# Performance work log

Measured on AMD Instinct MI355X. Metric: run time of the kernel, lower is better.

## Reference

```python
import jax, jax.numpy as jnp
import numpy as np

N_STEPS = 128        # params['n_steps']
NOISE_SCALE = 0.01   # params['noise_scale']
DIMS_X = 16
HID = 512
BATCH = 32768
DIMS_IN = 2 * DIMS_X + 1  # cond_x1=True: cat([t, x_t, x_1])


def _linear_init(key, fan_in, fan_out):
    # torch nn.Linear default: U(-1/sqrt(fan_in), 1/sqrt(fan_in))
    bound = 1.0 / np.sqrt(fan_in)
    kw, kb = jax.random.split(key)
    w = jax.random.uniform(kw, (fan_in, fan_out), jnp.float32, -bound, bound)
    b = jax.random.uniform(kb, (fan_out,), jnp.float32, -bound, bound)
    return w, b


def setup_inputs() -> dict:
    key = jax.random.key(0)
    ks = jax.random.split(key, 6)
    w0, b0 = _linear_init(ks[0], DIMS_IN, HID)
    w1, b1 = _linear_init(ks[1], HID, HID)
    w2, b2 = _linear_init(ks[2], HID, HID)
    w3, b3 = _linear_init(ks[3], HID, HID)
    w4, b4 = _linear_init(ks[4], HID, DIMS_X)
    x_1 = jax.random.normal(ks[5], (BATCH, DIMS_X), jnp.float32)
    return {"x_1": x_1, "w0": w0, "b0": b0, "w1": w1, "b1": b1,
            "w2": w2, "b2": b2, "w3": w3, "b3": b3, "w4": w4, "b4": b4}


def reference(x_1, w0, b0, w1, b1, w2, b2, w3, b3, w4, b4):
    dtype = x_1.dtype
    steps = jnp.linspace(1.0, 0.0, N_STEPS).astype(dtype)
    t_arr = steps[:-1]       # t
    tprev_arr = steps[1:]    # tprev (< t)
    noise_key = jax.random.key(42)
    ones_col = jnp.ones((x_1.shape[0], 1), dtype)

    def net(t, x_t):
        h = jnp.concatenate([t * ones_col, x_t, x_1], axis=-1)  # [B, 2*Dx+1]
        for w, b in ((w0, b0), (w1, b1), (w2, b2), (w3, b3)):
            h = jax.nn.relu(h @ w + b)
        return h @ w4 + b4  # [B, Dx]

    def body(x_t, inp):
        t, tprev, i = inp
        drift = net(t, x_t)
        pred_x0 = x_t - t * drift
        x_new = (t - tprev) / t * pred_x0 + tprev / t * x_t
        noise = jax.random.normal(jax.random.fold_in(noise_key, i), x_t.shape, dtype)
        x_new = x_new + jnp.sqrt(NOISE_SCALE * tprev * (t - tprev) / t) * noise
        return x_new, None

    x0 = jax.lax.stop_gradient(x_1)  # x_t = x_1.detach()
    x_final, _ = jax.lax.scan(body, x0, (t_arr, tprev_arr, jnp.arange(N_STEPS - 1)))
    return x_final
```

## Files before the change

kernel.cpp:

```cpp
#include <hip/hip_runtime.h>

typedef _Float16 f16;
typedef __attribute__((ext_vector_type(4))) _Float16 f16x4;
typedef __attribute__((ext_vector_type(8))) _Float16 f16x8;
typedef __attribute__((ext_vector_type(4))) float f32x4;
typedef __attribute__((ext_vector_type(16))) float f32x16;

#define HID 512
#define DIMS_X 16
#define NSTEPS 127
#define BM 128
#define BATCH 32768

#define OFF_W0 0
#define OFF_W1 32768
#define OFF_W2 (32768 + 262144)
#define OFF_W3 (32768 + 2 * 262144)
#define OFF_W4 (32768 + 3 * 262144)

__global__ void pack_w_kernel(const float* __restrict__ w, f16* __restrict__ out,
                              int K, int Kpad, int N) {
    int idx = blockIdx.x * blockDim.x + threadIdx.x;
    if (idx >= Kpad * N) return;
    int k = idx / N, n = idx - k * N;
    float v = (k < K) ? w[k * N + n] : 0.0f;
    out[(((k >> 3) * N) + n) * 8 + (k & 7)] = (f16)v;
}

__global__ void pack_w0_kernel(const float* __restrict__ w, f16* __restrict__ out) {
    int idx = blockIdx.x * blockDim.x + threadIdx.x;
    if (idx >= 64 * HID) return;
    int kn = idx / HID, n = idx - kn * HID;
    float v;
    if (kn < 32) v = w[(kn + 1) * HID + n];
    else if (kn == 32) v = w[n];
    else v = 0.0f;
    out[(((kn >> 3) * HID) + n) * 8 + (kn & 7)] = (f16)v;
}

__device__ __forceinline__ unsigned rotl32(unsigned x, int r) {
    return (x << r) | (x >> (32 - r));
}

__device__ __forceinline__ void threefry2x32(unsigned k0, unsigned k1,
                                             unsigned c0, unsigned c1,
                                             unsigned& o0, unsigned& o1) {
    unsigned ks2 = k0 ^ k1 ^ 0x1BD11BDAu;
    unsigned x0 = c0 + k0, x1 = c1 + k1;
#define TF_R(rot) { x0 += x1; x1 = rotl32(x1, rot); x1 ^= x0; }
    TF_R(13) TF_R(15) TF_R(26) TF_R(6)
    x0 += k1;  x1 += ks2 + 1u;
    TF_R(17) TF_R(29) TF_R(16) TF_R(24)
    x0 += ks2; x1 += k0 + 2u;
    TF_R(13) TF_R(15) TF_R(26) TF_R(6)
    x0 += k0;  x1 += k1 + 3u;
    TF_R(17) TF_R(29) TF_R(16) TF_R(24)
    x0 += k1;  x1 += ks2 + 4u;
    TF_R(13) TF_R(15) TF_R(26) TF_R(6)
    x0 += ks2; x1 += k0 + 5u;
#undef TF_R
    o0 = x0; o1 = x1;
}

__device__ __forceinline__ float erfinv_xla(float x) {
    float w = -log1pf(-x * x);
    float p;
    if (w < 5.0f) {
        w = w - 2.5f;
        p = 2.81022636e-08f;
        p = fmaf(p, w, 3.43273939e-07f);
        p = fmaf(p, w, -3.5233877e-06f);
        p = fmaf(p, w, -4.39150654e-06f);
        p = fmaf(p, w, 0.00021858087f);
        p = fmaf(p, w, -0.00125372503f);
        p = fmaf(p, w, -0.00417768164f);
        p = fmaf(p, w, 0.246640727f);
        p = fmaf(p, w, 1.50140941f);
    } else {
        w = sqrtf(w) - 3.0f;
        p = -0.000200214257f;
        p = fmaf(p, w, 0.000100950558f);
        p = fmaf(p, w, 0.00134934322f);
        p = fmaf(p, w, -0.00367342844f);
        p = fmaf(p, w, 0.00573950773f);
        p = fmaf(p, w, -0.0076224613f);
        p = fmaf(p, w, 0.00943887047f);
        p = fmaf(p, w, 1.00167406f);
        p = fmaf(p, w, 2.83297682f);
    }
    return p * x;
}

__device__ __forceinline__ unsigned lds_off(int row, int colByte) {
    return (unsigned)(row * 1024 + (colByte ^ ((row & 31) << 4)));
}

#define KC_BODY(kc, wc, wn, bc, bn, NCHUNK)                                           \
    {                                                                                 \
        if ((kc) + 1 < (NCHUNK)) {                                                    \
            const f16* wk = wbase + (size_t)((kc) + 1) * (2 * HID * 8);               \
            wn[0] = *(const f16x8*)(wk);                                              \
            wn[1] = *(const f16x8*)(wk + 256);                                        \
            _Pragma("unroll")                                                         \
            for (int tb = 0; tb < 4; ++tb)                                            \
                bn[tb] = *(const f16x8*)((const char*)act +                           \
                    lds_off(tb * 32 + l31, ((kc) + 1) * 32 + kh * 16));               \
        }                                                                             \
        _Pragma("unroll")                                                             \
        for (int t = 0; t < 2; ++t)                                                   \
            _Pragma("unroll")                                                         \
            for (int tb = 0; tb < 4; ++tb)                                            \
                acc[t][tb] = __builtin_amdgcn_mfma_f32_32x32x16_f16(                  \
                    wc[t], bc[tb], acc[t][tb], 0, 0, 0);                              \
    }

template <int NCHUNK>
__device__ __forceinline__ void layer_swapped(f16* act, const f16* __restrict__ Wp,
                                              const float* bias_l,
                                              int wv, int l31, int kh) {
    f32x16 acc[2][4];
#pragma unroll
    for (int t = 0; t < 2; ++t) {
        f32x4 bq0 = *(const f32x4*)(bias_l + wv * 64 + t * 32 + 0 + kh * 4);
        f32x4 bq1 = *(const f32x4*)(bias_l + wv * 64 + t * 32 + 8 + kh * 4);
        f32x4 bq2 = *(const f32x4*)(bias_l + wv * 64 + t * 32 + 16 + kh * 4);
        f32x4 bq3 = *(const f32x4*)(bias_l + wv * 64 + t * 32 + 24 + kh * 4);
        f32x16 bv;
#pragma unroll
        for (int r = 0; r < 4; ++r) {
            bv[r] = bq0[r]; bv[4 + r] = bq1[r]; bv[8 + r] = bq2[r]; bv[12 + r] = bq3[r];
        }
#pragma unroll
        for (int tb = 0; tb < 4; ++tb) acc[t][tb] = bv;
    }

    const f16* wbase = Wp + ((size_t)kh * HID + wv * 64 + l31) * 8;
    f16x8 wA[2], wB[2], bA[4], bB[4];
    wA[0] = *(const f16x8*)(wbase);
    wA[1] = *(const f16x8*)(wbase + 256);
#pragma unroll
    for (int tb = 0; tb < 4; ++tb)
        bA[tb] = *(const f16x8*)((const char*)act + lds_off(tb * 32 + l31, kh * 16));

#pragma unroll 1
    for (int kp = 0; kp < NCHUNK / 2; ++kp) {
        KC_BODY(2 * kp, wA, wB, bA, bB, NCHUNK)
        KC_BODY(2 * kp + 1, wB, wA, bB, bA, NCHUNK)
    }

    __syncthreads();
#pragma unroll
    for (int t = 0; t < 2; ++t)
#pragma unroll
        for (int tb = 0; tb < 4; ++tb) {
            int b = tb * 32 + l31;
#pragma unroll
            for (int q = 0; q < 4; ++q) {
                f16x4 v;
#pragma unroll
                for (int r = 0; r < 4; ++r)
                    v[r] = (f16)fmaxf(acc[t][tb][4 * q + r], 0.0f);
                int nb = (wv * 64 + t * 32 + q * 8 + kh * 4) * 2;
                *(f16x4*)((char*)act + lds_off(b, nb)) = v;
            }
        }
    __syncthreads();
}

__global__ __launch_bounds__(512, 2) void didi_main(
    const float* __restrict__ x1g,
    const float* __restrict__ b0g, const float* __restrict__ b1g,
    const float* __restrict__ b2g, const float* __restrict__ b3g,
    const float* __restrict__ b4g,
    const f16* __restrict__ wsp,
    float* __restrict__ outg) {
    __shared__ __align__(16) f16 act[BM * HID];
    __shared__ __align__(16) float bias_lds[4 * HID];

    const f16* W0p = wsp + OFF_W0;
    const f16* W1p = wsp + OFF_W1;
    const f16* W2p = wsp + OFF_W2;
    const f16* W3p = wsp + OFF_W3;
    const f16* W4p = wsp + OFF_W4;

    const int tid = threadIdx.x;
    const int wv = tid >> 6;
    const int ln = tid & 63;
    const int l31 = ln & 31;
    const int kh = ln >> 5;
    const int lk = ln >> 4;
    const int lc = ln & 15;
    const int rowBase = blockIdx.x * BM;

    for (int o = tid; o < HID; o += 512) {
        bias_lds[o] = b0g[o];
        bias_lds[HID + o] = b1g[o];
        bias_lds[2 * HID + o] = b2g[o];
        bias_lds[3 * HID + o] = b3g[o];
    }
    f32x4 bias4v = *(const f32x4*)(b4g + lk * 4);

    {
        f16x8 z = {};
        for (int o = tid; o < (BM * HID) / 8; o += 512)
            *(f16x8*)(act + o * 8) = z;
    }
    __syncthreads();

    f32x4 xr, x1r;
    {
        int grow = rowBase + wv * 16 + lc;
        x1r = *(const f32x4*)(x1g + grow * DIMS_X + lk * 4);
        xr = x1r;
        int lrow = wv * 16 + lc;
        f16x4 xf, x1f;
#pragma unroll
        for (int r = 0; r < 4; ++r) { xf[r] = (f16)xr[r]; x1f[r] = (f16)x1r[r]; }
        *(f16x4*)((char*)act + lds_off(lrow, lk * 8)) = xf;
        *(f16x4*)((char*)act + lds_off(lrow, 32 + lk * 8)) = x1f;
        if (lk == 0)
            *(f16*)((char*)act + lds_off(lrow, 64)) = (f16)1.0f;
    }
    __syncthreads();

    const float dstep = -1.0f / 127.0f;

#pragma unroll 1
    for (int i = 0; i < NSTEPS; ++i) {
        layer_swapped<4>(act, W0p, bias_lds, wv, l31, kh);
        layer_swapped<32>(act, W1p, bias_lds + HID, wv, l31, kh);
        layer_swapped<32>(act, W2p, bias_lds + 2 * HID, wv, l31, kh);
        layer_swapped<32>(act, W3p, bias_lds + 3 * HID, wv, l31, kh);

        float t  = 1.0f + (float)i * dstep;
        float tp = (i == NSTEPS - 1) ? 0.0f : 1.0f + (float)(i + 1) * dstep;

        {
            f32x4 acc4 = bias4v;
#pragma unroll 4
            for (int kc = 0; kc < 16; ++kc) {
                f16x8 w4fr = *(const f16x8*)(W4p + ((size_t)(kc * 4 + lk) * 16 + lc) * 8);
                f16x8 afr = *(const f16x8*)((const char*)act + lds_off(wv * 16 + lc, kc * 64 + lk * 16));
                acc4 = __builtin_amdgcn_mfma_f32_16x16x32_f16(w4fr, afr, acc4, 0, 0, 0);
            }
            float ca = (t - tp) / t;
            float cb = tp / t;
            float sig = sqrtf(((0.01f * tp) * (t - tp)) / t);
            unsigned fk0, fk1;
            threefry2x32(0u, 42u, 0u, (unsigned)i, fk0, fk1);
            int grow = rowBase + wv * 16 + lc;
            int lrow = wv * 16 + lc;
            f16x4 xf, x1f;
#pragma unroll
            for (int r = 0; r < 4; ++r) {
                float drift = acc4[r];
                unsigned flat = (unsigned)grow * 16u + (unsigned)(lk * 4 + r);
                unsigned o0, o1;
                threefry2x32(fk0, fk1, 0u, flat, o0, o1);
                unsigned bits = o0 ^ o1;
                float u01 = __uint_as_float((bits >> 9) | 0x3f800000u) - 1.0f;
                float u = u01 * 2.0f + (-0.99999994f);
                u = fmaxf(-0.99999994f, u);
                float nz = 1.4142135623730951f * erfinv_xla(u);
                float x = xr[r];
                float pred = x - t * drift;
                float xn = ca * pred + cb * x;
                xn = xn + sig * nz;
                xr[r] = xn;
                xf[r] = (f16)xn;
                x1f[r] = (f16)x1r[r];
            }
            *(f16x4*)((char*)act + lds_off(lrow, lk * 8)) = xf;
            *(f16x4*)((char*)act + lds_off(lrow, 32 + lk * 8)) = x1f;
            if (lk == 0)
                *(f16*)((char*)act + lds_off(lrow, 64)) = (f16)tp;
        }
        __syncthreads();
    }

    {
        int grow = rowBase + wv * 16 + lc;
        *(f32x4*)(outg + grow * DIMS_X + lk * 4) = xr;
    }
}

extern "C" void kernel_launch(void* const* d_in, const int* in_sizes, int n_in,
                              void* d_out, int out_size, void* d_ws, size_t ws_size,
                              hipStream_t stream) {
    const float* x1 = (const float*)d_in[0];
    const float* w0 = (const float*)d_in[1];
    const float* b0 = (const float*)d_in[2];
    const float* w1 = (const float*)d_in[3];
    const float* b1 = (const float*)d_in[4];
    const float* w2 = (const float*)d_in[5];
    const float* b2 = (const float*)d_in[6];
    const float* w3 = (const float*)d_in[7];
    const float* b3 = (const float*)d_in[8];
    const float* w4 = (const float*)d_in[9];
    const float* b4 = (const float*)d_in[10];
    f16* ws = (f16*)d_ws;

    hipLaunchKernelGGL(pack_w0_kernel, dim3(128), dim3(256), 0, stream, w0, ws + OFF_W0);
    hipLaunchKernelGGL(pack_w_kernel, dim3(1024), dim3(256), 0, stream, w1, ws + OFF_W1, 512, 512, 512);
    hipLaunchKernelGGL(pack_w_kernel, dim3(1024), dim3(256), 0, stream, w2, ws + OFF_W2, 512, 512, 512);
    hipLaunchKernelGGL(pack_w_kernel, dim3(1024), dim3(256), 0, stream, w3, ws + OFF_W3, 512, 512, 512);
    hipLaunchKernelGGL(pack_w_kernel, dim3(32), dim3(256), 0, stream, w4, ws + OFF_W4, 512, 512, 16);

    hipLaunchKernelGGL(didi_main, dim3(BATCH / BM), dim3(512), 0, stream,
                       x1, b0, b1, b2, b3, b4, (const f16*)ws, (float*)d_out);
}
```

Measured before the change: 6.268 ms.

## Overlap layer epilogue with own-chunk MMAs and stagger K order per wave

Each wave writes its ReLU outputs into the shared activation buffer. Without waiting at a barrier, it then runs the next layer's MMAs on the four K-chunks it just produced, using weights loaded before the epilogue. Only after that does it synchronise and process the remaining chunks in a wave-rotated order. This hides part of the epilogue and barrier latency behind tensor-core work and spreads LDS and weight accesses across waves; the output layer uses the same pattern. Activation fragments are no longer double-buffered in registers, which may expose LDS latency inside the main loop.

```diff
diff --git a/kernel.cpp b/kernel.cpp
--- a/kernel.cpp
+++ b/kernel.cpp
@@ -95,30 +95,26 @@
     return (unsigned)(row * 1024 + (colByte ^ ((row & 31) << 4)));
 }
 
-#define KC_BODY(kc, wc, wn, bc, bn, NCHUNK)                                           \
-    {                                                                                 \
-        if ((kc) + 1 < (NCHUNK)) {                                                    \
-            const f16* wk = wbase + (size_t)((kc) + 1) * (2 * HID * 8);               \
-            wn[0] = *(const f16x8*)(wk);                                              \
-            wn[1] = *(const f16x8*)(wk + 256);                                        \
-            _Pragma("unroll")                                                         \
-            for (int tb = 0; tb < 4; ++tb)                                            \
-                bn[tb] = *(const f16x8*)((const char*)act +                           \
-                    lds_off(tb * 32 + l31, ((kc) + 1) * 32 + kh * 16));               \
-        }                                                                             \
-        _Pragma("unroll")                                                             \
-        for (int t = 0; t < 2; ++t)                                                   \
-            _Pragma("unroll")                                                         \
-            for (int tb = 0; tb < 4; ++tb)                                            \
-                acc[t][tb] = __builtin_amdgcn_mfma_f32_32x32x16_f16(                  \
-                    wc[t], bc[tb], acc[t][tb], 0, 0, 0);                              \
-    }
-
-template <int NCHUNK>
-__device__ __forceinline__ void layer_swapped(f16* act, const f16* __restrict__ Wp,
-                                              const float* bias_l,
-                                              int wv, int l31, int kh) {
-    f32x16 acc[2][4];
+__device__ __forceinline__ void kc_mfma8(f32x16 (&acc)[2][4], const f16* act,
+                                         const f16x8& w0, const f16x8& w1,
+                                         int kc, int l31, int kh) {
+    unsigned colPart = (unsigned)((kc * 32 + kh * 16) ^ (l31 << 4));
+    f16x8 b0 = *(const f16x8*)((const char*)act + (unsigned)((0 * 32 + l31) * 1024) + colPart);
+    f16x8 b1 = *(const f16x8*)((const char*)act + (unsigned)((1 * 32 + l31) * 1024) + colPart);
+    f16x8 b2 = *(const f16x8*)((const char*)act + (unsigned)((2 * 32 + l31) * 1024) + colPart);
+    f16x8 b3 = *(const f16x8*)((const char*)act + (unsigned)((3 * 32 + l31) * 1024) + colPart);
+    acc[0][0] = __builtin_amdgcn_mfma_f32_32x32x16_f16(w0, b0, acc[0][0], 0, 0, 0);
+    acc[0][1] = __builtin_amdgcn_mfma_f32_32x32x16_f16(w0, b1, acc[0][1], 0, 0, 0);
+    acc[0][2] = __builtin_amdgcn_mfma_f32_32x32x16_f16(w0, b2, acc[0][2], 0, 0, 0);
+    acc[0][3] = __builtin_amdgcn_mfma_f32_32x32x16_f16(w0, b3, acc[0][3], 0, 0, 0);
+    acc[1][0] = __builtin_amdgcn_mfma_f32_32x32x16_f16(w1, b0, acc[1][0], 0, 0, 0);
+    acc[1][1] = __builtin_amdgcn_mfma_f32_32x32x16_f16(w1, b1, acc[1][1], 0, 0, 0);
+    acc[1][2] = __builtin_amdgcn_mfma_f32_32x32x16_f16(w1, b2, acc[1][2], 0, 0, 0);
+    acc[1][3] = __builtin_amdgcn_mfma_f32_32x32x16_f16(w1, b3, acc[1][3], 0, 0, 0);
+}
+
+__device__ __forceinline__ void init_acc(f32x16 (&acc)[2][4], const float* bias_l,
+                                         int wv, int kh) {
 #pragma unroll
     for (int t = 0; t < 2; ++t) {
         f32x4 bq0 = *(const f32x4*)(bias_l + wv * 64 + t * 32 + 0 + kh * 4);
@@ -133,22 +129,10 @@
 #pragma unroll
         for (int tb = 0; tb < 4; ++tb) acc[t][tb] = bv;
     }
-
-    const f16* wbase = Wp + ((size_t)kh * HID + wv * 64 + l31) * 8;
-    f16x8 wA[2], wB[2], bA[4], bB[4];
-    wA[0] = *(const f16x8*)(wbase);
-    wA[1] = *(const f16x8*)(wbase + 256);
-#pragma unroll
-    for (int tb = 0; tb < 4; ++tb)
-        bA[tb] = *(const f16x8*)((const char*)act + lds_off(tb * 32 + l31, kh * 16));
-
-#pragma unroll 1
-    for (int kp = 0; kp < NCHUNK / 2; ++kp) {
-        KC_BODY(2 * kp, wA, wB, bA, bB, NCHUNK)
-        KC_BODY(2 * kp + 1, wB, wA, bB, bA, NCHUNK)
-    }
-
-    __syncthreads();
+}
+
+__device__ __forceinline__ void epi_relu(f32x16 (&acc)[2][4], f16* act,
+                                         int wv, int l31, int kh) {
 #pragma unroll
     for (int t = 0; t < 2; ++t)
 #pragma unroll
@@ -164,7 +148,52 @@
                 *(f16x4*)((char*)act + lds_off(b, nb)) = v;
             }
         }
-    __syncthreads();
+}
+
+__device__ __forceinline__ void load_w4(f16x8 (&wE)[8], const f16* __restrict__ Wp,
+                                        int wv4, int l31, int kh) {
+    const f16* wbase = Wp + ((size_t)kh * HID + wv4 * 16 + l31) * 8;
+#pragma unroll
+    for (int j = 0; j < 4; ++j) {
+        const f16* wk = wbase + (size_t)(wv4 + j) * 8192;
+        wE[2 * j] = *(const f16x8*)wk;
+        wE[2 * j + 1] = *(const f16x8*)(wk + 256);
+    }
+}
+
+__device__ __forceinline__ void early4(f32x16 (&acc)[2][4], const f16* act,
+                                       const f16x8 (&wE)[8], int wv4, int l31, int kh) {
+#pragma unroll
+    for (int j = 0; j < 4; ++j)
+        kc_mfma8(acc, act, wE[2 * j], wE[2 * j + 1], wv4 + j, l31, kh);
+}
+
+__device__ __forceinline__ void hidden_main(f32x16 (&acc)[2][4], const f16* act,
+                                            const f16* __restrict__ Wp,
+                                            int wv4, int l31, int kh) {
+    const f16* wbase = Wp + ((size_t)kh * HID + wv4 * 16 + l31) * 8;
+    f16x8 wA0, wA1, wB0, wB1;
+    {
+        int kc = (wv4 + 4) & 31;
+        const f16* wk = wbase + (size_t)kc * 8192;
+        wA0 = *(const f16x8*)wk; wA1 = *(const f16x8*)(wk + 256);
+    }
+#pragma unroll 1
+    for (int kp = 0; kp < 14; ++kp) {
+        int j0 = 4 + 2 * kp;
+        int kc1 = (wv4 + j0 + 1) & 31;
+        {
+            const f16* wk = wbase + (size_t)kc1 * 8192;
+            wB0 = *(const f16x8*)wk; wB1 = *(const f16x8*)(wk + 256);
+        }
+        kc_mfma8(acc, act, wA0, wA1, (wv4 + j0) & 31, l31, kh);
+        int kc2 = (wv4 + j0 + 2) & 31;
+        {
+            const f16* wk = wbase + (size_t)kc2 * 8192;
+            wA0 = *(const f16x8*)wk; wA1 = *(const f16x8*)(wk + 256);
+        }
+        kc_mfma8(acc, act, wB0, wB1, kc1, l31, kh);
+    }
 }
 
 __global__ __launch_bounds__(512, 2) void didi_main(
@@ -190,6 +219,8 @@
     const int kh = ln >> 5;
     const int lk = ln >> 4;
     const int lc = ln & 15;
+    const int wv4 = wv * 4;
+    const int wv2 = wv * 2;
     const int rowBase = blockIdx.x * BM;
 
     for (int o = tid; o < HID; o += 512) {
@@ -224,25 +255,65 @@
     __syncthreads();
 
     const float dstep = -1.0f / 127.0f;
+    f32x16 acc[2][4];
+    f16x8 wE[8];
 
 #pragma unroll 1
     for (int i = 0; i < NSTEPS; ++i) {
-        layer_swapped<4>(act, W0p, bias_lds, wv, l31, kh);
-        layer_swapped<32>(act, W1p, bias_lds + HID, wv, l31, kh);
-        layer_swapped<32>(act, W2p, bias_lds + 2 * HID, wv, l31, kh);
-        layer_swapped<32>(act, W3p, bias_lds + 3 * HID, wv, l31, kh);
+        init_acc(acc, bias_lds, wv, kh);
+        {
+            const f16* wbase = W0p + ((size_t)kh * HID + wv4 * 16 + l31) * 8;
+#pragma unroll
+            for (int kc = 0; kc < 4; ++kc) {
+                const f16* wk = wbase + (size_t)kc * 8192;
+                f16x8 w0 = *(const f16x8*)wk, w1 = *(const f16x8*)(wk + 256);
+                kc_mfma8(acc, act, w0, w1, kc, l31, kh);
+            }
+        }
+        __syncthreads();
+        load_w4(wE, W1p, wv4, l31, kh);
+        epi_relu(acc, act, wv, l31, kh);
+        init_acc(acc, bias_lds + HID, wv, kh);
+        early4(acc, act, wE, wv4, l31, kh);
+        __syncthreads();
+        hidden_main(acc, act, W1p, wv4, l31, kh);
+        __syncthreads();
+        load_w4(wE, W2p, wv4, l31, kh);
+        epi_relu(acc, act, wv, l31, kh);
+        init_acc(acc, bias_lds + 2 * HID, wv, kh);
+        early4(acc, act, wE, wv4, l31, kh);
+        __syncthreads();
+        hidden_main(acc, act, W2p, wv4, l31, kh);
+        __syncthreads();
+        load_w4(wE, W3p, wv4, l31, kh);
+        epi_relu(acc, act, wv, l31, kh);
+        init_acc(acc, bias_lds + 3 * HID, wv, kh);
+        early4(acc, act, wE, wv4, l31, kh);
+        __syncthreads();
+        hidden_main(acc, act, W3p, wv4, l31, kh);
+        __syncthreads();
+        epi_relu(acc, act, wv, l31, kh);
 
         float t  = 1.0f + (float)i * dstep;
         float tp = (i == NSTEPS - 1) ? 0.0f : 1.0f + (float)(i + 1) * dstep;
 
+        f32x4 acc4 = bias4v;
+#pragma unroll
+        for (int j = 0; j < 2; ++j) {
+            int kc = wv2 + j;
+            f16x8 w4fr = *(const f16x8*)(W4p + ((size_t)(kc * 4 + lk) * 16 + lc) * 8);
+            f16x8 afr = *(const f16x8*)((const char*)act + lds_off(wv * 16 + lc, kc * 64 + lk * 16));
+            acc4 = __builtin_amdgcn_mfma_f32_16x16x32_f16(w4fr, afr, acc4, 0, 0, 0);
+        }
+        __syncthreads();
+#pragma unroll
+        for (int j = 2; j < 16; ++j) {
+            int kc = wv2 + j; if (kc >= 16) kc -= 16;
+            f16x8 w4fr = *(const f16x8*)(W4p + ((size_t)(kc * 4 + lk) * 16 + lc) * 8);
+            f16x8 afr = *(const f16x8*)((const char*)act + lds_off(wv * 16 + lc, kc * 64 + lk * 16));
+            acc4 = __builtin_amdgcn_mfma_f32_16x16x32_f16(w4fr, afr, acc4, 0, 0, 0);
+        }
         {
-            f32x4 acc4 = bias4v;
-#pragma unroll 4
-            for (int kc = 0; kc < 16; ++kc) {
-                f16x8 w4fr = *(const f16x8*)(W4p + ((size_t)(kc * 4 + lk) * 16 + lc) * 8);
-                f16x8 afr = *(const f16x8*)((const char*)act + lds_off(wv * 16 + lc, kc * 64 + lk * 16));
-                acc4 = __builtin_amdgcn_mfma_f32_16x16x32_f16(w4fr, afr, acc4, 0, 0, 0);
-            }
             float ca = (t - tp) / t;
             float cb = tp / t;
             float sig = sqrtf(((0.01f * tp) * (t - tp)) / t);
```

Measured after the change: 10.40 ms. +66.0%, slower.
